# Performance work log

Measured on AMD Instinct MI355X. Metric: run time of the kernel, lower is better.

## Reference

```python
import jax, jax.numpy as jnp
import numpy as np

B, S, D, H, HD = 2, 2048, 1024, 16, 64
SCALE = HD ** (-0.5)

def setup_inputs() -> dict:
    key = jax.random.key(0)
    ks = jax.random.split(key, 11)
    f = jax.random.normal
    return {
        "K_in": f(ks[0], (B, S, D), jnp.float32),
        "V_in": f(ks[1], (B, S, D), jnp.float32),
        "Q_in": f(ks[2], (B, S, D), jnp.float32),
        "Wk": f(ks[3], (H, D, HD), jnp.float32) * 0.02,
        "bk": f(ks[4], (H, HD), jnp.float32) * 0.02,
        "Wq": f(ks[5], (H, D, HD), jnp.float32) * 0.02,
        "bq": f(ks[6], (H, HD), jnp.float32) * 0.02,
        "Wv": f(ks[7], (H, D, HD), jnp.float32) * 0.02,
        "bv": f(ks[8], (H, HD), jnp.float32) * 0.02,
        "Wp": f(ks[9], (D, D), jnp.float32) * 0.02,
        "bp": f(ks[10], (D,), jnp.float32) * 0.02,
    }

def reference(K_in, V_in, Q_in, Wk, bk, Wq, bq, Wv, bv, Wp, bp):
    # Per-head linear projections (batched over heads): [B,H,S,HD]
    K = jnp.einsum('bsd,hde->bhse', K_in, Wk) + bk[None, :, None, :]
    Q = jnp.einsum('bsd,hde->bhse', Q_in, Wq) + bq[None, :, None, :]
    V = jnp.einsum('bsd,hde->bhse', V_in, Wv) + bv[None, :, None, :]
    # Attention scores [B,H,S,S], softmax over keys
    W = jax.nn.softmax(jnp.einsum('bhqe,bhke->bhqk', Q, K) * SCALE, axis=-1)
    val = jnp.einsum('bhqk,bhke->bhqe', W, V)            # [B,H,S,HD]
    # Concatenate heads along feature dim -> [B,S,H*HD] = [B,S,D]
    concat = jnp.transpose(val, (0, 2, 1, 3)).reshape(K_in.shape[0], K_in.shape[1], -1)
    return concat @ Wp.T + bp
```

## Files before the change

### kernel.cpp

```cpp
#include <hip/hip_runtime.h>
#include <hip/hip_bf16.h>
#include <math.h>

typedef float f32x4 __attribute__((ext_vector_type(4)));
typedef short s16x8 __attribute__((ext_vector_type(8)));
typedef unsigned short us16x4 __attribute__((ext_vector_type(4)));
typedef unsigned short us16x8 __attribute__((ext_vector_type(8)));
typedef unsigned int u32x2 __attribute__((ext_vector_type(2)));

#define MFMA16(a, b, c) __builtin_amdgcn_mfma_f32_16x16x32_bf16(a, b, c, 0, 0, 0)

static constexpr int B_ = 2, S_ = 2048, D_ = 1024, H_ = 16, HD_ = 64;
static constexpr float QSCALE = 0.125f * 1.44269504088896340736f;

__device__ __forceinline__ unsigned short f2bf(float f) {
    unsigned int u = __builtin_bit_cast(unsigned int, f);
    u += 0x7fffu + ((u >> 16) & 1);
    return (unsigned short)(u >> 16);
}

#if defined(__has_builtin) && __has_builtin(__builtin_amdgcn_cvt_pk_bf16_f32)
typedef __bf16 bf16x2v __attribute__((ext_vector_type(2)));
__device__ __forceinline__ unsigned int pk_bf16(float a, float b) {
    return __builtin_bit_cast(unsigned int, __builtin_amdgcn_cvt_pk_bf16_f32(a, b));
}
#else
__device__ __forceinline__ unsigned int pk_bf16(float a, float b) {
    return ((unsigned int)f2bf(a)) | (((unsigned int)f2bf(b)) << 16);
}
#endif

__device__ __forceinline__ void glds16(const unsigned short* g, unsigned short* l) {
    __builtin_amdgcn_global_load_lds(
        (const __attribute__((address_space(1))) void*)g,
        (__attribute__((address_space(3))) void*)l, 16, 0, 0);
}

__global__ __launch_bounds__(256) void conv3(const float* __restrict__ s0,
                                             const float* __restrict__ s1,
                                             const float* __restrict__ s2,
                                             unsigned short* __restrict__ d0,
                                             unsigned short* __restrict__ d1,
                                             unsigned short* __restrict__ d2) {
    const int z = blockIdx.z;
    const float* src = (z == 0) ? s0 : (z == 1) ? s1 : s2;
    unsigned short* dst = (z == 0) ? d0 : (z == 1) ? d1 : d2;
    int i = (blockIdx.x * 256 + threadIdx.x) * 8;
    f32x4 a = *(const f32x4*)&src[i];
    f32x4 b = *(const f32x4*)&src[i + 4];
    s16x8 o;
#pragma unroll
    for (int j = 0; j < 4; j++) { o[j] = (short)f2bf(a[j]); o[4 + j] = (short)f2bf(b[j]); }
    *(s16x8*)&dst[i] = o;
}

__global__ __launch_bounds__(256) void conv_bf16(const float* __restrict__ src,
                                                 unsigned short* __restrict__ dst) {
    int i = (blockIdx.x * 256 + threadIdx.x) * 8;
    f32x4 a = *(const f32x4*)&src[i];
    f32x4 b = *(const f32x4*)&src[i + 4];
    s16x8 o;
#pragma unroll
    for (int j = 0; j < 4; j++) { o[j] = (short)f2bf(a[j]); o[4 + j] = (short)f2bf(b[j]); }
    *(s16x8*)&dst[i] = o;
}

__global__ __launch_bounds__(256) void transpose_w3(const float* __restrict__ W0,
                                                    const float* __restrict__ W1,
                                                    const float* __restrict__ W2,
                                                    unsigned short* __restrict__ Wt3) {
    const int z = blockIdx.z;
    const float* W = (z == 0) ? W0 : (z == 1) ? W1 : W2;
    unsigned short* dst = Wt3 + ((size_t)z << 20);
    const int h = blockIdx.x >> 2, dg = blockIdx.x & 3;
    const int lane = threadIdx.x & 63, w = threadIdx.x >> 6;
    const float* Wh = W + ((size_t)h << 16);
#pragma unroll
    for (int it = 0; it < 8; it++) {
        int d0 = dg * 256 + it * 32 + w * 8;
        us16x8 o;
#pragma unroll
        for (int j = 0; j < 8; j++) o[j] = f2bf(Wh[(d0 + j) * 64 + lane]);
        *(us16x8*)&dst[(size_t)(h * 64 + lane) * 1024 + d0] = o;
    }
}

__device__ __forceinline__ void gemm_core128(const unsigned short* __restrict__ A,
                                             const unsigned short* __restrict__ Bt,
                                             unsigned short* As, unsigned short* Bs,
                                             int m0, int n0, f32x4 acc[4][4]) {
    const int tid = threadIdx.x;
    const int lane = tid & 63;
    const int w = tid >> 6, wm = w & 1, wn = w >> 1;
    const int l16 = lane & 15, quad = lane >> 4;
    const int srow = tid >> 3;
    const int sg = (tid & 7) ^ (srow & 7);
    const unsigned short* Ag = A + (size_t)(m0 + srow) * 1024 + sg * 8;
    const unsigned short* Bg = Bt + (size_t)(n0 + srow) * 1024 + sg * 8;
    unsigned short* Al = As + tid * 8;
    unsigned short* Bl = Bs + tid * 8;
    const int xo = (l16 & 7);

    for (int k0 = 0; k0 < 1024; k0 += 64) {
        __syncthreads();
#pragma unroll
        for (int c = 0; c < 4; c++) {
            glds16(Ag + (size_t)c * 32 * 1024 + k0, Al + c * 2048);
            glds16(Bg + (size_t)c * 32 * 1024 + k0, Bl + c * 2048);
        }
        __syncthreads();
#pragma unroll
        for (int kc = 0; kc < 2; kc++) {
            s16x8 bf[4];
#pragma unroll
            for (int nt = 0; nt < 4; nt++)
                bf[nt] = *(const s16x8*)&Bs[(wn * 64 + nt * 16 + l16) * 64 +
                                            (((kc * 4 + quad) ^ xo) * 8)];
#pragma unroll
            for (int mt = 0; mt < 4; mt++) {
                s16x8 af = *(const s16x8*)&As[(wm * 64 + mt * 16 + l16) * 64 +
                                              (((kc * 4 + quad) ^ xo) * 8)];
#pragma unroll
                for (int nt = 0; nt < 4; nt++)
                    acc[mt][nt] = MFMA16(af, bf[nt], acc[mt][nt]);
            }
        }
    }
}

__global__ __launch_bounds__(256) void gemm_qkv(const unsigned short* __restrict__ Qc,
                                                const unsigned short* __restrict__ Kc,
                                                const unsigned short* __restrict__ Vc,
                                                const unsigned short* __restrict__ Wt3,
                                                const float* __restrict__ bq,
                                                const float* __restrict__ bk,
                                                const float* __restrict__ bv,
                                                unsigned short* __restrict__ Qr,
                                                unsigned short* __restrict__ Kr,
                                                unsigned short* __restrict__ Vt) {
    __shared__ unsigned short As[128 * 64];
    __shared__ unsigned short Bs[128 * 64];
    const int flat = blockIdx.x + (blockIdx.y << 3) + (blockIdx.z << 8);
    const int wid = (flat & 7) * 96 + (flat >> 3);
    const int z = wid >> 8;
    const int by = (wid & 255) >> 3;
    const int bx = wid & 7;
    const unsigned short* A = (z == 0) ? Qc : (z == 1) ? Kc : Vc;
    const unsigned short* Bt = Wt3 + ((size_t)z << 20);
    const float* bias = (z == 0) ? bq : (z == 1) ? bk : bv;
    const int m0 = by * 128, n0 = bx * 128;

    f32x4 acc[4][4] = {};
    gemm_core128(A, Bt, As, Bs, m0, n0, acc);

    const int tid = threadIdx.x;
    const int lane = tid & 63, w = tid >> 6;
    const int wm = w & 1, wn = w >> 1;
    const int l16 = lane & 15, quad = lane >> 4;
    const float scl = (z == 0) ? QSCALE : 1.0f;

    __syncthreads();
    unsigned short* T = ((w < 2) ? As : Bs) + (w & 1) * 4096;
#pragma unroll
    for (int mt = 0; mt < 4; mt++)
#pragma unroll
        for (int nt = 0; nt < 4; nt++) {
            int nl = nt * 16 + l16;
            float bsv = bias[n0 + wn * 64 + nl];
#pragma unroll
            for (int r = 0; r < 4; r++) {
                int ml = mt * 16 + quad * 4 + r;
                unsigned short val = f2bf((acc[mt][nt][r] + bsv) * scl);
                int row = (z == 2) ? nl : ml;
                int col = (z == 2) ? ml : nl;
                T[row * 64 + (((col >> 3) ^ (row & 7)) * 8) + (col & 7)] = val;
            }
        }
#pragma unroll
    for (int it = 0; it < 8; it++) {
        int rr = it * 8 + (lane >> 3);
        int g = lane & 7;
        us16x8 vv = *(const us16x8*)&T[rr * 64 + ((g ^ (rr & 7)) * 8)];
        if (z == 2) {
            int n = n0 + wn * 64 + rr;
            int mb = m0 + wm * 64 + g * 8;
            int b = mb >> 11, s = mb & 2047;
            *(us16x8*)&Vt[(((size_t)(b * H_ + (n >> 6))) * HD_ + (n & 63)) * S_ + s] = vv;
        } else {
            unsigned short* dst = z ? Kr : Qr;
            *(us16x8*)&dst[(size_t)(m0 + wm * 64 + rr) * 1024 + n0 + wn * 64 + g * 8] = vv;
        }
    }
}

__global__ __launch_bounds__(256) void gemm_out(const unsigned short* __restrict__ A,
                                                const unsigned short* __restrict__ Bt,
                                                const float* __restrict__ bias,
                                                float* __restrict__ C) {
    __shared__ unsigned short As[128 * 64];
    __shared__ unsigned short Bs[64 * 64];
    const int tid = threadIdx.x;
    const int lane = tid & 63;
    const int w = tid >> 6, wm = w & 1, wn = w >> 1;
    const int l16 = lane & 15, quad = lane >> 4;
    const int flat = blockIdx.x + (blockIdx.y << 4);
    const int wid = (flat & 7) * 64 + (flat >> 3);
    const int m0 = (wid >> 4) * 128, n0 = (wid & 15) * 64;
    const int srow = tid >> 3;
    const int sg = (tid & 7) ^ (srow & 7);
    const unsigned short* Ag = A + (size_t)(m0 + srow) * 1024 + sg * 8;
    const unsigned short* Bg = Bt + (size_t)(n0 + srow) * 1024 + sg * 8;
    unsigned short* Al = As + tid * 8;
    unsigned short* Bl = Bs + tid * 8;
    const int xo = l16 & 7;

    f32x4 acc[4][2] = {};
    for (int k0 = 0; k0 < 1024; k0 += 64) {
        __syncthreads();
#pragma unroll
        for (int c = 0; c < 4; c++)
            glds16(Ag + (size_t)c * 32 * 1024 + k0, Al + c * 2048);
#pragma unroll
        for (int c = 0; c < 2; c++)
            glds16(Bg + (size_t)c * 32 * 1024 + k0, Bl + c * 2048);
        __syncthreads();
#pragma unroll
        for (int kc = 0; kc < 2; kc++) {
            s16x8 bf[2];
#pragma unroll
            for (int nt = 0; nt < 2; nt++)
                bf[nt] = *(const s16x8*)&Bs[(wn * 32 + nt * 16 + l16) * 64 +
                                            (((kc * 4 + quad) ^ xo) * 8)];
#pragma unroll
            for (int mt = 0; mt < 4; mt++) {
                s16x8 af = *(const s16x8*)&As[(wm * 64 + mt * 16 + l16) * 64 +
                                              (((kc * 4 + quad) ^ xo) * 8)];
#pragma unroll
                for (int nt = 0; nt < 2; nt++)
                    acc[mt][nt] = MFMA16(af, bf[nt], acc[mt][nt]);
            }
        }
    }
    const int lq = quad;
#pragma unroll
    for (int mt = 0; mt < 4; mt++)
#pragma unroll
        for (int nt = 0; nt < 2; nt++)
#pragma unroll
            for (int r = 0; r < 4; r++) {
                int mg = m0 + wm * 64 + mt * 16 + lq * 4 + r;
                int ng = n0 + wn * 32 + nt * 16 + l16;
                C[(size_t)mg * 1024 + ng] = acc[mt][nt][r] + bias[ng];
            }
}

__global__ __launch_bounds__(256) void flash_attn(const unsigned short* __restrict__ Qr,
                                                  const unsigned short* __restrict__ Kr,
                                                  const unsigned short* __restrict__ Vt,
                                                  unsigned short* __restrict__ Cc) {
    __shared__ unsigned short Ks[2][64 * 64];
    __shared__ unsigned short Vs[64 * 64];
    constexpr int LDT = 72;
    __shared__ unsigned short P4[4][16 * LDT];

    const int tid = threadIdx.x;
    const int lane = tid & 63, w = tid >> 6;
    const int l16 = lane & 15, quad = lane >> 4;
    const int bh = blockIdx.x, q0 = blockIdx.y * 64;
    const int b = bh >> 4, h = bh & 15;
    const int s_q = q0 + w * 16 + l16;

    const unsigned short* Qp = Qr + ((size_t)(b * S_ + s_q)) * D_ + h * HD_;

    const int srow = tid >> 3;
    const int sg = (tid & 7) ^ (srow & 7);
    const unsigned short* kg = Kr + ((size_t)(b * S_ + srow)) * D_ + h * HD_ + sg * 8;
    const unsigned short* vg = Vt + (((size_t)(b * H_ + h)) * HD_ + srow) * S_ + sg * 8;
    unsigned short* Vl = Vs + tid * 8;
    unsigned short* Pw = P4[w];
    const int pbase = l16 * LDT + quad * 4;
    const int xo = l16 & 7;

    glds16(kg, &Ks[0][tid * 8]);
    glds16(kg + (size_t)32 * D_, &Ks[0][tid * 8 + 2048]);
    kg += (size_t)64 * D_;

    s16x8 aq0 = *(const s16x8*)&Qp[quad * 8];
    s16x8 aq1 = *(const s16x8*)&Qp[32 + quad * 8];

    float l_part = 0.f;
    f32x4 o[4] = {};
    const f32x4 z4 = {0.f, 0.f, 0.f, 0.f};

    asm volatile("s_waitcnt vmcnt(0) lgkmcnt(0)\n\ts_barrier" ::: "memory");

    int cur = 0;
    for (int t = 0; t < 32; ++t) {
        const int last = (t == 31);
        glds16(vg, Vl);
        glds16(vg + (size_t)32 * S_, Vl + 2048);
        vg += 64;
        if (!last) {
            unsigned short* Kn = &Ks[cur ^ 1][tid * 8];
            glds16(kg, Kn);
            glds16(kg + (size_t)32 * D_, Kn + 2048);
            kg += (size_t)64 * D_;
        }

        const unsigned short* Kc_ = &Ks[cur][0];
        __builtin_amdgcn_s_setprio(1);
#pragma unroll
        for (int g = 0; g < 4; g++) {
            int row = g * 16 + l16;
            s16x8 kb0 = *(const s16x8*)&Kc_[row * 64 + ((quad ^ xo) * 8)];
            s16x8 kb1 = *(const s16x8*)&Kc_[row * 64 + (((4 + quad) ^ xo) * 8)];
            f32x4 sc = MFMA16(kb0, aq0, z4);
            sc = MFMA16(kb1, aq1, sc);
            float e0 = exp2f(sc[0]), e1 = exp2f(sc[1]);
            float e2 = exp2f(sc[2]), e3 = exp2f(sc[3]);
            l_part += (e0 + e1) + (e2 + e3);
            u32x2 pv;
            pv[0] = pk_bf16(e0, e1);
            pv[1] = pk_bf16(e2, e3);
            *(u32x2*)&Pw[pbase + g * 16] = pv;
        }
        __builtin_amdgcn_s_setprio(0);
        s16x8 pB0 = *(const s16x8*)&Pw[l16 * LDT + quad * 8];
        s16x8 pB1 = *(const s16x8*)&Pw[l16 * LDT + 32 + quad * 8];

        if (!last)
            asm volatile("s_waitcnt vmcnt(2)\n\ts_barrier" ::: "memory");
        else
            asm volatile("s_waitcnt vmcnt(0)\n\ts_barrier" ::: "memory");

        __builtin_amdgcn_s_setprio(1);
#pragma unroll
        for (int tt = 0; tt < 4; tt++) {
            int row = tt * 16 + l16;
            s16x8 v0 = *(const s16x8*)&Vs[row * 64 + ((quad ^ xo) * 8)];
            s16x8 v1 = *(const s16x8*)&Vs[row * 64 + (((4 + quad) ^ xo) * 8)];
            o[tt] = MFMA16(v0, pB0, o[tt]);
            o[tt] = MFMA16(v1, pB1, o[tt]);
        }
        __builtin_amdgcn_s_setprio(0);
        asm volatile("s_waitcnt vmcnt(0) lgkmcnt(0)\n\ts_barrier" ::: "memory");
        cur ^= 1;
    }

    float l = l_part;
    l += __shfl_xor(l, 16);
    l += __shfl_xor(l, 32);
    float rinv = 1.0f / l;
    unsigned short* Cp = Cc + ((size_t)(b * S_ + s_q)) * D_ + h * HD_;
#pragma unroll
    for (int t = 0; t < 4; t++) {
        u32x2 ov;
        ov[0] = pk_bf16(o[t][0] * rinv, o[t][1] * rinv);
        ov[1] = pk_bf16(o[t][2] * rinv, o[t][3] * rinv);
        *(u32x2*)&Cp[t * 16 + quad * 4] = ov;
    }
}

extern "C" void kernel_launch(void* const* d_in, const int* in_sizes, int n_in,
                              void* d_out, int out_size, void* d_ws, size_t ws_size,
                              hipStream_t stream) {
    const float* K_in = (const float*)d_in[0];
    const float* V_in = (const float*)d_in[1];
    const float* Q_in = (const float*)d_in[2];
    const float* Wk   = (const float*)d_in[3];
    const float* bk   = (const float*)d_in[4];
    const float* Wq   = (const float*)d_in[5];
    const float* bq   = (const float*)d_in[6];
    const float* Wv   = (const float*)d_in[7];
    const float* bv   = (const float*)d_in[8];
    const float* Wp   = (const float*)d_in[9];
    const float* bp   = (const float*)d_in[10];

    unsigned short* ws16 = (unsigned short*)d_ws;
    const size_t MC = 1u << 20;
    unsigned short* Qc  = ws16;
    unsigned short* Kc  = Qc + 4 * MC;
    unsigned short* Vc  = Kc + 4 * MC;
    unsigned short* Wt3 = Vc + 4 * MC;
    unsigned short* Qr  = Wt3 + 3 * MC;
    unsigned short* Kr  = Qr + 4 * MC;
    unsigned short* Vt  = Kr + 4 * MC;
    unsigned short* Cc  = Qc;
    unsigned short* Wpb = Wt3;

    conv3<<<dim3(2048, 1, 3), 256, 0, stream>>>(Q_in, K_in, V_in, Qc, Kc, Vc);
    transpose_w3<<<dim3(64, 1, 3), 256, 0, stream>>>(Wq, Wk, Wv, Wt3);

    gemm_qkv<<<dim3(8, 32, 3), 256, 0, stream>>>(Qc, Kc, Vc, Wt3, bq, bk, bv, Qr, Kr, Vt);

    conv_bf16<<<512, 256, 0, stream>>>(Wp, Wpb);

    flash_attn<<<dim3(32, 32), 256, 0, stream>>>(Qr, Kr, Vt, Cc);

    gemm_out<<<dim3(16, 32), 256, 0, stream>>>(Cc, Wpb, bp, (float*)d_out);
}
```

Measured before the change: 253.7 us.

## Fuse fp32-to-bf16 input conversion into QKV and output GEMM tile loads

Removes the separate conv3 and conv_bf16 kernels. The QKV GEMM now loads fp32 activations straight into LDS and packs them to bf16 at fragment-read time, and the output GEMM does the same for Wp. This drops two launches and the write and re-read of bf16 copies. In exchange, the GEMM tiles read twice as many global bytes per K step (each QKV N-tile block rereads the fp32 A rows), use more LDS, and spend ALU on conversion inside the inner loop.

Result: no change. 253.3 us (-0.2%).

```diff
diff --git a/kernel.cpp b/kernel.cpp
--- a/kernel.cpp
+++ b/kernel.cpp
@@ -36,33 +36,10 @@
         (__attribute__((address_space(3))) void*)l, 16, 0, 0);
 }
 
-__global__ __launch_bounds__(256) void conv3(const float* __restrict__ s0,
-                                             const float* __restrict__ s1,
-                                             const float* __restrict__ s2,
-                                             unsigned short* __restrict__ d0,
-                                             unsigned short* __restrict__ d1,
-                                             unsigned short* __restrict__ d2) {
-    const int z = blockIdx.z;
-    const float* src = (z == 0) ? s0 : (z == 1) ? s1 : s2;
-    unsigned short* dst = (z == 0) ? d0 : (z == 1) ? d1 : d2;
-    int i = (blockIdx.x * 256 + threadIdx.x) * 8;
-    f32x4 a = *(const f32x4*)&src[i];
-    f32x4 b = *(const f32x4*)&src[i + 4];
-    s16x8 o;
-#pragma unroll
-    for (int j = 0; j < 4; j++) { o[j] = (short)f2bf(a[j]); o[4 + j] = (short)f2bf(b[j]); }
-    *(s16x8*)&dst[i] = o;
-}
-
-__global__ __launch_bounds__(256) void conv_bf16(const float* __restrict__ src,
-                                                 unsigned short* __restrict__ dst) {
-    int i = (blockIdx.x * 256 + threadIdx.x) * 8;
-    f32x4 a = *(const f32x4*)&src[i];
-    f32x4 b = *(const f32x4*)&src[i + 4];
-    s16x8 o;
-#pragma unroll
-    for (int j = 0; j < 4; j++) { o[j] = (short)f2bf(a[j]); o[4 + j] = (short)f2bf(b[j]); }
-    *(s16x8*)&dst[i] = o;
+__device__ __forceinline__ void glds16f(const float* g, float* l) {
+    __builtin_amdgcn_global_load_lds(
+        (const __attribute__((address_space(1))) void*)g,
+        (__attribute__((address_space(3))) void*)l, 16, 0, 0);
 }
 
 __global__ __launch_bounds__(256) void transpose_w3(const float* __restrict__ W0,
@@ -85,52 +62,9 @@
     }
 }
 
-__device__ __forceinline__ void gemm_core128(const unsigned short* __restrict__ A,
-                                             const unsigned short* __restrict__ Bt,
-                                             unsigned short* As, unsigned short* Bs,
-                                             int m0, int n0, f32x4 acc[4][4]) {
-    const int tid = threadIdx.x;
-    const int lane = tid & 63;
-    const int w = tid >> 6, wm = w & 1, wn = w >> 1;
-    const int l16 = lane & 15, quad = lane >> 4;
-    const int srow = tid >> 3;
-    const int sg = (tid & 7) ^ (srow & 7);
-    const unsigned short* Ag = A + (size_t)(m0 + srow) * 1024 + sg * 8;
-    const unsigned short* Bg = Bt + (size_t)(n0 + srow) * 1024 + sg * 8;
-    unsigned short* Al = As + tid * 8;
-    unsigned short* Bl = Bs + tid * 8;
-    const int xo = (l16 & 7);
-
-    for (int k0 = 0; k0 < 1024; k0 += 64) {
-        __syncthreads();
-#pragma unroll
-        for (int c = 0; c < 4; c++) {
-            glds16(Ag + (size_t)c * 32 * 1024 + k0, Al + c * 2048);
-            glds16(Bg + (size_t)c * 32 * 1024 + k0, Bl + c * 2048);
-        }
-        __syncthreads();
-#pragma unroll
-        for (int kc = 0; kc < 2; kc++) {
-            s16x8 bf[4];
-#pragma unroll
-            for (int nt = 0; nt < 4; nt++)
-                bf[nt] = *(const s16x8*)&Bs[(wn * 64 + nt * 16 + l16) * 64 +
-                                            (((kc * 4 + quad) ^ xo) * 8)];
-#pragma unroll
-            for (int mt = 0; mt < 4; mt++) {
-                s16x8 af = *(const s16x8*)&As[(wm * 64 + mt * 16 + l16) * 64 +
-                                              (((kc * 4 + quad) ^ xo) * 8)];
-#pragma unroll
-                for (int nt = 0; nt < 4; nt++)
-                    acc[mt][nt] = MFMA16(af, bf[nt], acc[mt][nt]);
-            }
-        }
-    }
-}
-
-__global__ __launch_bounds__(256) void gemm_qkv(const unsigned short* __restrict__ Qc,
-                                                const unsigned short* __restrict__ Kc,
-                                                const unsigned short* __restrict__ Vc,
+__global__ __launch_bounds__(256) void gemm_qkv(const float* __restrict__ Qf,
+                                                const float* __restrict__ Kf,
+                                                const float* __restrict__ Vf,
                                                 const unsigned short* __restrict__ Wt3,
                                                 const float* __restrict__ bq,
                                                 const float* __restrict__ bk,
@@ -138,29 +72,71 @@
                                                 unsigned short* __restrict__ Qr,
                                                 unsigned short* __restrict__ Kr,
                                                 unsigned short* __restrict__ Vt) {
-    __shared__ unsigned short As[128 * 64];
+    __shared__ float Asf[128 * 64];
     __shared__ unsigned short Bs[128 * 64];
     const int flat = blockIdx.x + (blockIdx.y << 3) + (blockIdx.z << 8);
     const int wid = (flat & 7) * 96 + (flat >> 3);
     const int z = wid >> 8;
     const int by = (wid & 255) >> 3;
     const int bx = wid & 7;
-    const unsigned short* A = (z == 0) ? Qc : (z == 1) ? Kc : Vc;
-    const unsigned short* Bt = Wt3 + ((size_t)z << 20);
+    const float* A = (z == 0) ? Qf : (z == 1) ? Kf : Vf;
     const float* bias = (z == 0) ? bq : (z == 1) ? bk : bv;
     const int m0 = by * 128, n0 = bx * 128;
 
+    const int tid = threadIdx.x;
+    const int lane = tid & 63;
+    const int w = tid >> 6, wm = w & 1, wn = w >> 1;
+    const int l16 = lane & 15, quad = lane >> 4;
+    const int arow = tid >> 4;
+    const int su = (tid & 15) ^ arow;
+    const float* Ag = A + (size_t)(m0 + arow) * 1024 + su * 4;
+    float* Alf = Asf + tid * 4;
+    const int srow = tid >> 3;
+    const int sg = (tid & 7) ^ (srow & 7);
+    const unsigned short* Bg = Wt3 + ((size_t)z << 20) + (size_t)(n0 + srow) * 1024 + sg * 8;
+    unsigned short* Bl = Bs + tid * 8;
+    const int xo8 = l16 & 7;
+
     f32x4 acc[4][4] = {};
-    gemm_core128(A, Bt, As, Bs, m0, n0, acc);
-
-    const int tid = threadIdx.x;
-    const int lane = tid & 63, w = tid >> 6;
-    const int wm = w & 1, wn = w >> 1;
-    const int l16 = lane & 15, quad = lane >> 4;
+    for (int k0 = 0; k0 < 1024; k0 += 64) {
+        __syncthreads();
+#pragma unroll
+        for (int c = 0; c < 8; c++)
+            glds16f(Ag + (size_t)c * 16 * 1024 + k0, Alf + c * 1024);
+#pragma unroll
+        for (int c = 0; c < 4; c++)
+            glds16(Bg + (size_t)c * 32 * 1024 + k0, Bl + c * 2048);
+        __syncthreads();
+#pragma unroll
+        for (int kc = 0; kc < 2; kc++) {
+            s16x8 bf[4];
+#pragma unroll
+            for (int nt = 0; nt < 4; nt++)
+                bf[nt] = *(const s16x8*)&Bs[(wn * 64 + nt * 16 + l16) * 64 +
+                                            (((kc * 4 + quad) ^ xo8) * 8)];
+#pragma unroll
+            for (int mt = 0; mt < 4; mt++) {
+                const int row = wm * 64 + mt * 16 + l16;
+                const int u = kc * 8 + quad * 2;
+                const int e = row & 15;
+                f32x4 lo = *(const f32x4*)&Asf[row * 64 + ((u ^ e) * 4)];
+                f32x4 hi = *(const f32x4*)&Asf[row * 64 + (((u + 1) ^ e) * 4)];
+                s16x8 af;
+                ((unsigned int*)&af)[0] = pk_bf16(lo[0], lo[1]);
+                ((unsigned int*)&af)[1] = pk_bf16(lo[2], lo[3]);
+                ((unsigned int*)&af)[2] = pk_bf16(hi[0], hi[1]);
+                ((unsigned int*)&af)[3] = pk_bf16(hi[2], hi[3]);
+#pragma unroll
+                for (int nt = 0; nt < 4; nt++)
+                    acc[mt][nt] = MFMA16(af, bf[nt], acc[mt][nt]);
+            }
+        }
+    }
+
     const float scl = (z == 0) ? QSCALE : 1.0f;
 
     __syncthreads();
-    unsigned short* T = ((w < 2) ? As : Bs) + (w & 1) * 4096;
+    unsigned short* T = ((unsigned short*)Asf) + w * 4096;
 #pragma unroll
     for (int mt = 0; mt < 4; mt++)
 #pragma unroll
@@ -194,11 +170,11 @@
 }
 
 __global__ __launch_bounds__(256) void gemm_out(const unsigned short* __restrict__ A,
-                                                const unsigned short* __restrict__ Bt,
+                                                const float* __restrict__ Wp,
                                                 const float* __restrict__ bias,
                                                 float* __restrict__ C) {
     __shared__ unsigned short As[128 * 64];
-    __shared__ unsigned short Bs[64 * 64];
+    __shared__ float Bsf[64 * 64];
     const int tid = threadIdx.x;
     const int lane = tid & 63;
     const int w = tid >> 6, wm = w & 1, wn = w >> 1;
@@ -209,10 +185,12 @@
     const int srow = tid >> 3;
     const int sg = (tid & 7) ^ (srow & 7);
     const unsigned short* Ag = A + (size_t)(m0 + srow) * 1024 + sg * 8;
-    const unsigned short* Bg = Bt + (size_t)(n0 + srow) * 1024 + sg * 8;
     unsigned short* Al = As + tid * 8;
-    unsigned short* Bl = Bs + tid * 8;
-    const int xo = l16 & 7;
+    const int brow = tid >> 4;
+    const int su = (tid & 15) ^ brow;
+    const float* Bg = Wp + (size_t)(n0 + brow) * 1024 + su * 4;
+    float* Blf = Bsf + tid * 4;
+    const int xo8 = l16 & 7;
 
     f32x4 acc[4][2] = {};
     for (int k0 = 0; k0 < 1024; k0 += 64) {
@@ -221,20 +199,28 @@
         for (int c = 0; c < 4; c++)
             glds16(Ag + (size_t)c * 32 * 1024 + k0, Al + c * 2048);
 #pragma unroll
-        for (int c = 0; c < 2; c++)
-            glds16(Bg + (size_t)c * 32 * 1024 + k0, Bl + c * 2048);
+        for (int c = 0; c < 4; c++)
+            glds16f(Bg + (size_t)c * 16 * 1024 + k0, Blf + c * 1024);
         __syncthreads();
 #pragma unroll
         for (int kc = 0; kc < 2; kc++) {
             s16x8 bf[2];
 #pragma unroll
-            for (int nt = 0; nt < 2; nt++)
-                bf[nt] = *(const s16x8*)&Bs[(wn * 32 + nt * 16 + l16) * 64 +
-                                            (((kc * 4 + quad) ^ xo) * 8)];
+            for (int nt = 0; nt < 2; nt++) {
+                const int row = wn * 32 + nt * 16 + l16;
+                const int u = kc * 8 + quad * 2;
+                const int e = row & 15;
+                f32x4 lo = *(const f32x4*)&Bsf[row * 64 + ((u ^ e) * 4)];
+                f32x4 hi = *(const f32x4*)&Bsf[row * 64 + (((u + 1) ^ e) * 4)];
+                ((unsigned int*)&bf[nt])[0] = pk_bf16(lo[0], lo[1]);
+                ((unsigned int*)&bf[nt])[1] = pk_bf16(lo[2], lo[3]);
+                ((unsigned int*)&bf[nt])[2] = pk_bf16(hi[0], hi[1]);
+                ((unsigned int*)&bf[nt])[3] = pk_bf16(hi[2], hi[3]);
+            }
 #pragma unroll
             for (int mt = 0; mt < 4; mt++) {
                 s16x8 af = *(const s16x8*)&As[(wm * 64 + mt * 16 + l16) * 64 +
-                                              (((kc * 4 + quad) ^ xo) * 8)];
+                                              (((kc * 4 + quad) ^ xo8) * 8)];
 #pragma unroll
                 for (int nt = 0; nt < 2; nt++)
                     acc[mt][nt] = MFMA16(af, bf[nt], acc[mt][nt]);
@@ -378,24 +364,18 @@
 
     unsigned short* ws16 = (unsigned short*)d_ws;
     const size_t MC = 1u << 20;
-    unsigned short* Qc  = ws16;
-    unsigned short* Kc  = Qc + 4 * MC;
-    unsigned short* Vc  = Kc + 4 * MC;
-    unsigned short* Wt3 = Vc + 4 * MC;
+    unsigned short* Wt3 = ws16;
     unsigned short* Qr  = Wt3 + 3 * MC;
     unsigned short* Kr  = Qr + 4 * MC;
     unsigned short* Vt  = Kr + 4 * MC;
-    unsigned short* Cc  = Qc;
-    unsigned short* Wpb = Wt3;
-
-    conv3<<<dim3(2048, 1, 3), 256, 0, stream>>>(Q_in, K_in, V_in, Qc, Kc, Vc);
+    unsigned short* Cc  = Vt + 4 * MC;
+
     transpose_w3<<<dim3(64, 1, 3), 256, 0, stream>>>(Wq, Wk, Wv, Wt3);
 
-    gemm_qkv<<<dim3(8, 32, 3), 256, 0, stream>>>(Qc, Kc, Vc, Wt3, bq, bk, bv, Qr, Kr, Vt);
-
-    conv_bf16<<<512, 256, 0, stream>>>(Wp, Wpb);
+    gemm_qkv<<<dim3(8, 32, 3), 256, 0, stream>>>(Q_in, K_in, V_in, Wt3, bq, bk, bv,
+                                                 Qr, Kr, Vt);
 
     flash_attn<<<dim3(32, 32), 256, 0, stream>>>(Qr, Kr, Vt, Cc);
 
-    gemm_out<<<dim3(16, 32), 256, 0, stream>>>(Cc, Wpb, bp, (float*)d_out);
-}
+    gemm_out<<<dim3(16, 32), 256, 0, stream>>>(Cc, Wp, bp, (float*)d_out);
+}
```

## Double-buffer LDS tiles in QKV and output projection GEMMs

Applied to the files above, without the earlier changes.

Both projection GEMMs now hold two LDS buffers and prefetch the next K-tile with direct global-to-LDS loads while MFMAs run on the current tile. The two barriers per iteration become one raw waitcnt+barrier, and wave priority is raised around the MFMA block. This hides global load latency behind compute, at the cost of double the LDS per block, which may reduce occupancy. The epilogue staging buffer is re-pointed into the enlarged As array.

Result: no change. 251.3 us (-0.9%).

```diff
diff --git a/kernel.cpp b/kernel.cpp
--- a/kernel.cpp
+++ b/kernel.cpp
@@ -85,49 +85,6 @@
     }
 }
 
-__device__ __forceinline__ void gemm_core128(const unsigned short* __restrict__ A,
-                                             const unsigned short* __restrict__ Bt,
-                                             unsigned short* As, unsigned short* Bs,
-                                             int m0, int n0, f32x4 acc[4][4]) {
-    const int tid = threadIdx.x;
-    const int lane = tid & 63;
-    const int w = tid >> 6, wm = w & 1, wn = w >> 1;
-    const int l16 = lane & 15, quad = lane >> 4;
-    const int srow = tid >> 3;
-    const int sg = (tid & 7) ^ (srow & 7);
-    const unsigned short* Ag = A + (size_t)(m0 + srow) * 1024 + sg * 8;
-    const unsigned short* Bg = Bt + (size_t)(n0 + srow) * 1024 + sg * 8;
-    unsigned short* Al = As + tid * 8;
-    unsigned short* Bl = Bs + tid * 8;
-    const int xo = (l16 & 7);
-
-    for (int k0 = 0; k0 < 1024; k0 += 64) {
-        __syncthreads();
-#pragma unroll
-        for (int c = 0; c < 4; c++) {
-            glds16(Ag + (size_t)c * 32 * 1024 + k0, Al + c * 2048);
-            glds16(Bg + (size_t)c * 32 * 1024 + k0, Bl + c * 2048);
-        }
-        __syncthreads();
-#pragma unroll
-        for (int kc = 0; kc < 2; kc++) {
-            s16x8 bf[4];
-#pragma unroll
-            for (int nt = 0; nt < 4; nt++)
-                bf[nt] = *(const s16x8*)&Bs[(wn * 64 + nt * 16 + l16) * 64 +
-                                            (((kc * 4 + quad) ^ xo) * 8)];
-#pragma unroll
-            for (int mt = 0; mt < 4; mt++) {
-                s16x8 af = *(const s16x8*)&As[(wm * 64 + mt * 16 + l16) * 64 +
-                                              (((kc * 4 + quad) ^ xo) * 8)];
-#pragma unroll
-                for (int nt = 0; nt < 4; nt++)
-                    acc[mt][nt] = MFMA16(af, bf[nt], acc[mt][nt]);
-            }
-        }
-    }
-}
-
 __global__ __launch_bounds__(256) void gemm_qkv(const unsigned short* __restrict__ Qc,
                                                 const unsigned short* __restrict__ Kc,
                                                 const unsigned short* __restrict__ Vc,
@@ -138,8 +95,8 @@
                                                 unsigned short* __restrict__ Qr,
                                                 unsigned short* __restrict__ Kr,
                                                 unsigned short* __restrict__ Vt) {
-    __shared__ unsigned short As[128 * 64];
-    __shared__ unsigned short Bs[128 * 64];
+    __shared__ unsigned short As[2][128 * 64];
+    __shared__ unsigned short Bs[2][128 * 64];
     const int flat = blockIdx.x + (blockIdx.y << 3) + (blockIdx.z << 8);
     const int wid = (flat & 7) * 96 + (flat >> 3);
     const int z = wid >> 8;
@@ -150,17 +107,63 @@
     const float* bias = (z == 0) ? bq : (z == 1) ? bk : bv;
     const int m0 = by * 128, n0 = bx * 128;
 
+    const int tid = threadIdx.x;
+    const int lane = tid & 63;
+    const int w = tid >> 6, wm = w & 1, wn = w >> 1;
+    const int l16 = lane & 15, quad = lane >> 4;
+    const int srow = tid >> 3;
+    const int sg = (tid & 7) ^ (srow & 7);
+    const unsigned short* Ag = A + (size_t)(m0 + srow) * 1024 + sg * 8;
+    const unsigned short* Bg = Bt + (size_t)(n0 + srow) * 1024 + sg * 8;
+    const int xo = l16 & 7;
+
     f32x4 acc[4][4] = {};
-    gemm_core128(A, Bt, As, Bs, m0, n0, acc);
-
-    const int tid = threadIdx.x;
-    const int lane = tid & 63, w = tid >> 6;
-    const int wm = w & 1, wn = w >> 1;
-    const int l16 = lane & 15, quad = lane >> 4;
+
+#pragma unroll
+    for (int c = 0; c < 4; c++) {
+        glds16(Ag + (size_t)c * 32 * 1024, &As[0][tid * 8 + c * 2048]);
+        glds16(Bg + (size_t)c * 32 * 1024, &Bs[0][tid * 8 + c * 2048]);
+    }
+    asm volatile("s_waitcnt vmcnt(0)\n\ts_barrier" ::: "memory");
+
+    int cur = 0;
+    for (int t = 0; t < 16; ++t) {
+        if (t < 15) {
+            const int k0n = (t + 1) * 64;
+#pragma unroll
+            for (int c = 0; c < 4; c++) {
+                glds16(Ag + (size_t)c * 32 * 1024 + k0n, &As[cur ^ 1][tid * 8 + c * 2048]);
+                glds16(Bg + (size_t)c * 32 * 1024 + k0n, &Bs[cur ^ 1][tid * 8 + c * 2048]);
+            }
+        }
+        const unsigned short* Ac = &As[cur][0];
+        const unsigned short* Bc = &Bs[cur][0];
+        __builtin_amdgcn_s_setprio(1);
+#pragma unroll
+        for (int kc = 0; kc < 2; kc++) {
+            s16x8 bf[4];
+#pragma unroll
+            for (int nt = 0; nt < 4; nt++)
+                bf[nt] = *(const s16x8*)&Bc[(wn * 64 + nt * 16 + l16) * 64 +
+                                            (((kc * 4 + quad) ^ xo) * 8)];
+#pragma unroll
+            for (int mt = 0; mt < 4; mt++) {
+                s16x8 af = *(const s16x8*)&Ac[(wm * 64 + mt * 16 + l16) * 64 +
+                                              (((kc * 4 + quad) ^ xo) * 8)];
+#pragma unroll
+                for (int nt = 0; nt < 4; nt++)
+                    acc[mt][nt] = MFMA16(af, bf[nt], acc[mt][nt]);
+            }
+        }
+        __builtin_amdgcn_s_setprio(0);
+        asm volatile("s_waitcnt vmcnt(0)\n\ts_barrier" ::: "memory");
+        cur ^= 1;
+    }
+
     const float scl = (z == 0) ? QSCALE : 1.0f;
 
     __syncthreads();
-    unsigned short* T = ((w < 2) ? As : Bs) + (w & 1) * 4096;
+    unsigned short* T = ((unsigned short*)As) + w * 4096;
 #pragma unroll
     for (int mt = 0; mt < 4; mt++)
 #pragma unroll
@@ -197,8 +200,8 @@
                                                 const unsigned short* __restrict__ Bt,
                                                 const float* __restrict__ bias,
                                                 float* __restrict__ C) {
-    __shared__ unsigned short As[128 * 64];
-    __shared__ unsigned short Bs[64 * 64];
+    __shared__ unsigned short As[2][128 * 64];
+    __shared__ unsigned short Bs[2][64 * 64];
     const int tid = threadIdx.x;
     const int lane = tid & 63;
     const int w = tid >> 6, wm = w & 1, wn = w >> 1;
@@ -210,36 +213,51 @@
     const int sg = (tid & 7) ^ (srow & 7);
     const unsigned short* Ag = A + (size_t)(m0 + srow) * 1024 + sg * 8;
     const unsigned short* Bg = Bt + (size_t)(n0 + srow) * 1024 + sg * 8;
-    unsigned short* Al = As + tid * 8;
-    unsigned short* Bl = Bs + tid * 8;
     const int xo = l16 & 7;
 
     f32x4 acc[4][2] = {};
-    for (int k0 = 0; k0 < 1024; k0 += 64) {
-        __syncthreads();
-#pragma unroll
-        for (int c = 0; c < 4; c++)
-            glds16(Ag + (size_t)c * 32 * 1024 + k0, Al + c * 2048);
-#pragma unroll
-        for (int c = 0; c < 2; c++)
-            glds16(Bg + (size_t)c * 32 * 1024 + k0, Bl + c * 2048);
-        __syncthreads();
+
+#pragma unroll
+    for (int c = 0; c < 4; c++)
+        glds16(Ag + (size_t)c * 32 * 1024, &As[0][tid * 8 + c * 2048]);
+#pragma unroll
+    for (int c = 0; c < 2; c++)
+        glds16(Bg + (size_t)c * 32 * 1024, &Bs[0][tid * 8 + c * 2048]);
+    asm volatile("s_waitcnt vmcnt(0)\n\ts_barrier" ::: "memory");
+
+    int cur = 0;
+    for (int t = 0; t < 16; ++t) {
+        if (t < 15) {
+            const int k0n = (t + 1) * 64;
+#pragma unroll
+            for (int c = 0; c < 4; c++)
+                glds16(Ag + (size_t)c * 32 * 1024 + k0n, &As[cur ^ 1][tid * 8 + c * 2048]);
+#pragma unroll
+            for (int c = 0; c < 2; c++)
+                glds16(Bg + (size_t)c * 32 * 1024 + k0n, &Bs[cur ^ 1][tid * 8 + c * 2048]);
+        }
+        const unsigned short* Ac = &As[cur][0];
+        const unsigned short* Bc = &Bs[cur][0];
+        __builtin_amdgcn_s_setprio(1);
 #pragma unroll
         for (int kc = 0; kc < 2; kc++) {
             s16x8 bf[2];
 #pragma unroll
             for (int nt = 0; nt < 2; nt++)
-                bf[nt] = *(const s16x8*)&Bs[(wn * 32 + nt * 16 + l16) * 64 +
+                bf[nt] = *(const s16x8*)&Bc[(wn * 32 + nt * 16 + l16) * 64 +
                                             (((kc * 4 + quad) ^ xo) * 8)];
 #pragma unroll
             for (int mt = 0; mt < 4; mt++) {
-                s16x8 af = *(const s16x8*)&As[(wm * 64 + mt * 16 + l16) * 64 +
+                s16x8 af = *(const s16x8*)&Ac[(wm * 64 + mt * 16 + l16) * 64 +
                                               (((kc * 4 + quad) ^ xo) * 8)];
 #pragma unroll
                 for (int nt = 0; nt < 2; nt++)
                     acc[mt][nt] = MFMA16(af, bf[nt], acc[mt][nt]);
             }
         }
+        __builtin_amdgcn_s_setprio(0);
+        asm volatile("s_waitcnt vmcnt(0)\n\ts_barrier" ::: "memory");
+        cur ^= 1;
     }
     const int lq = quad;
 #pragma unroll
```
